# Performance work log

Hardware: AMD Instinct MI355X
Metric: run time of the kernel (lower is better)

## Reference

```python
import jax, jax.numpy as jnp
import numpy as np

NUM_NODES = 94
SEQ_LEN = 784
OUT_CLASSES = 10
ALPHA = 0.5
GAMMA = 0.1
OMEGA = 2.0 * np.pi / 28.0
H = 1.0
INV_SQRT_N = 1.0 / np.sqrt(NUM_NODES)


def _xavier(key, shape):
    fan_in, fan_out = shape[1], shape[0]
    limit = np.sqrt(6.0 / (fan_in + fan_out))
    return jax.random.uniform(key, shape, jnp.float32, -limit, limit)


def setup_inputs() -> dict:
    key = jax.random.key(0)
    k_in, k_ih, k_hh, k_ro = jax.random.split(key, 4)
    batch = 1024
    return {
        "input_sequence": jax.random.normal(k_in, (batch, SEQ_LEN), jnp.float32),
        "w_ih": _xavier(k_ih, (NUM_NODES, 1)),   # Linear(1 -> N) weight
        "b_ih": jnp.zeros((NUM_NODES,), jnp.float32),
        "w_hh": _xavier(k_hh, (NUM_NODES, NUM_NODES)),  # Linear(N -> N) weight
        "b_hh": jnp.zeros((NUM_NODES,), jnp.float32),
        "w_ro": _xavier(k_ro, (OUT_CLASSES, NUM_NODES)),  # readout weight
        "b_ro": jnp.zeros((OUT_CLASSES,), jnp.float32),
    }


def reference(input_sequence, w_ih, b_ih, w_hh, b_hh, w_ro, b_ro):
    batch = input_sequence.shape[0]
    # precompute external drive for all steps: [T, B, N]
    # W_ih(s_t) with input_dim=1 is an outer product: s_t * w_ih[:,0] + b_ih
    s = input_sequence.T  # [T, B]
    w_ih_vec = w_ih[:, 0]  # [N]

    def step(carry, s_t):
        x, y = carry
        I_ext = s_t[:, None] * w_ih_vec[None, :] + b_ih  # [B, N]
        I_rec = y @ w_hh.T + b_hh                        # [B, N]
        A = (I_ext + I_rec) * INV_SQRT_N
        accel = ALPHA * jnp.tanh(A) - 2.0 * GAMMA * y - (OMEGA ** 2) * x
        x_new = x + H * y
        y_new = y + H * accel
        return (x_new, y_new), None

    x0 = jnp.zeros((batch, NUM_NODES), jnp.float32)
    y0 = jnp.zeros((batch, NUM_NODES), jnp.float32)
    (x_final, _), _ = jax.lax.scan(step, (x0, y0), s)
    return x_final @ w_ro.T + b_ro  # [B, 10]
```

## Files before the change

### kernel.cpp

```cpp
#include <hip/hip_runtime.h>
#include <math.h>

#define NUM_NODES 94
#define SEQ_LEN 784
#define OUT_CLASSES 10
#define EPB 16
#define NW 6
#define SP 788
#define YHALF 1664

#define TWO_GAMMA 0.2f
#define OM2 0.0503551324598949f
#define INV_SQRT_N 0.103142124625879
#define LOG2E 1.4426950408889634
#define WSCALE ((float)(2.0 * INV_SQRT_N * LOG2E))

typedef _Float16 half8 __attribute__((ext_vector_type(8)));
typedef _Float16 half4 __attribute__((ext_vector_type(4)));
typedef _Float16 half2v __attribute__((ext_vector_type(2)));
typedef float    floatx4 __attribute__((ext_vector_type(4)));
typedef float    f2 __attribute__((ext_vector_type(2)));

__global__
__attribute__((amdgpu_flat_work_group_size(NW*64, NW*64)))
void horn_kernel(
    const float* __restrict__ input,
    const float* __restrict__ w_ih,
    const float* __restrict__ b_ih,
    const float* __restrict__ w_hh,
    const float* __restrict__ b_hh,
    const float* __restrict__ w_ro,
    const float* __restrict__ b_ro,
    float* __restrict__ out)
{
    __shared__ __align__(16) float    sinl[EPB * SP];
    __shared__ __align__(16) _Float16 ybuf[2][YHALF];

    const int tid  = threadIdx.x;
    const int w    = tid >> 6;
    const int lane = tid & 63;
    const int e    = lane & 15;
    const int h    = lane >> 4;
    const int bb   = blockIdx.x;

    const int  T        = w;
    const bool duty     = (w == 3 && h == 0);
    const bool tailmask = (w == 5 && h == 3);

    const int eoff = 104 * e + 4 * (e >> 3);

    {
        const floatx4* in4 = (const floatx4*)(input + (size_t)bb * EPB * SEQ_LEN);
        for (int idx = tid; idx < EPB * (SEQ_LEN / 4); idx += NW * 64) {
            int ee = idx / (SEQ_LEN / 4);
            int cc = idx - ee * (SEQ_LEN / 4);
            *(floatx4*)&sinl[ee * SP + 4 * cc] = in4[ee * (SEQ_LEN / 4) + cc];
        }
    }
    for (int i = tid; i < (2 * YHALF) / 2; i += NW * 64) ((float*)ybuf)[i] = 0.0f;

    const int arow = 16 * T + e;
    half8 a0, a1, a2;
    #pragma unroll
    for (int i = 0; i < 8; ++i) {
        const int k = 8 * h + i;
        float v0 = 0.0f, v1 = 0.0f, v2 = 0.0f;
        if (arow < NUM_NODES) {
            v0 = w_hh[arow * NUM_NODES + k] * WSCALE;
            if (k + 32 < NUM_NODES) v1 = w_hh[arow * NUM_NODES + k + 32] * WSCALE;
            const int k2 = k + 64;
            if      (k2 <  NUM_NODES) v2 = w_hh[arow * NUM_NODES + k2] * WSCALE;
            else if (k2 == NUM_NODES) v2 = w_ih[arow] * WSCALE;
            else                      v2 = (b_ih[arow] + b_hh[arow]) * WSCALE;
        }
        a0[i] = (_Float16)v0; a1[i] = (_Float16)v1; a2[i] = (_Float16)v2;
    }

    f2 x01 = {0,0}, x23 = {0,0}, y01 = {0,0}, y23 = {0,0};

    const floatx4 zf4 = {0,0,0,0};
    const f2 no2 = {-OM2, -OM2};
    const f2 p82 = {1.0f - TWO_GAMMA, 1.0f - TWO_GAMMA};
    const f2 h05 = {0.5f, 0.5f};

    __syncthreads();

    if (tid < EPB) {
        const int eo = 104 * tid + 4 * (tid >> 3);
        const float s0 = input[((size_t)bb * EPB + tid) * SEQ_LEN];
        half2v v0; v0[0] = (_Float16)s0; v0[1] = (_Float16)1.0f;
        half2v v1; v1[0] = (_Float16)0.0f; v1[1] = (_Float16)1.0f;
        *(half2v*)&ybuf[0][eo + NUM_NODES] = v0;
        *(half2v*)&ybuf[1][eo + NUM_NODES] = v1;
    }
    __syncthreads();

    #define HSTEP(RP, WP, T_) do {                                                 \
        const _Float16* Yb = &ybuf[RP][eoff + 8 * h];                              \
        half4 l0 = *(const half4*)(Yb);                                            \
        half4 u0 = *(const half4*)(Yb + 4);                                        \
        half4 l1 = *(const half4*)(Yb + 32);                                       \
        half4 u1 = *(const half4*)(Yb + 36);                                       \
        half4 l2 = *(const half4*)(Yb + 64);                                       \
        half4 u2 = *(const half4*)(Yb + 68);                                       \
                                \
        f2 q01 = no2 * x01 + h05;  q01 = p82 * y01 + q01;                          \
        f2 q23 = no2 * x23 + h05;  q23 = p82 * y23 + q23;                          \
        x01 += y01;  x23 += y23;                                                   \
        float snext = 0.0f;                                                        \
        if (duty) {                                                                \
            const int tn = ((T_) + 1 < SEQ_LEN) ? (T_) + 1 : (SEQ_LEN - 1);        \
            snext = sinl[e * SP + tn];                                             \
        }                                                                          \
        half8 B0 = __builtin_shufflevector(l0, u0, 0, 1, 2, 3, 4, 5, 6, 7);        \
        half8 B1 = __builtin_shufflevector(l1, u1, 0, 1, 2, 3, 4, 5, 6, 7);        \
        half8 B2 = __builtin_shufflevector(l2, u2, 0, 1, 2, 3, 4, 5, 6, 7);        \
        floatx4 d0 = __builtin_amdgcn_mfma_f32_16x16x32_f16(a0, B0, zf4, 0, 0, 0); \
        floatx4 d1 = __builtin_amdgcn_mfma_f32_16x16x32_f16(a1, B1, zf4, 0, 0, 0); \
        floatx4 d2 = __builtin_amdgcn_mfma_f32_16x16x32_f16(a2, B2, zf4, 0, 0, 0); \
        floatx4 d = (d0 + d1) + d2;    \
        f2 r01, r23;                                                               \
        r01[0] = __builtin_amdgcn_rcpf(__builtin_amdgcn_exp2f(d[0]) + 1.0f);       \
        r01[1] = __builtin_amdgcn_rcpf(__builtin_amdgcn_exp2f(d[1]) + 1.0f);       \
        r23[0] = __builtin_amdgcn_rcpf(__builtin_amdgcn_exp2f(d[2]) + 1.0f);       \
        r23[1] = __builtin_amdgcn_rcpf(__builtin_amdgcn_exp2f(d[3]) + 1.0f);       \
        y01 = q01 - r01;  y23 = q23 - r23;                                         \
        half4 yh;                                                                  \
        yh[0] = (_Float16)y01[0]; yh[1] = (_Float16)y01[1];                        \
        yh[2] = (_Float16)y23[0]; yh[3] = (_Float16)y23[1];                        \
        if (tailmask) {                                                            \
            half2v yt; yt[0] = yh[0]; yt[1] = yh[1];          \
            *(half2v*)&ybuf[WP][eoff + 92] = yt;                                   \
        } else {                                                                   \
            *(half4*)&ybuf[WP][eoff + 16 * T + 4 * h] = yh;                        \
        }                                                                          \
        if (duty) {                                                                \
            half2v sv; sv[0] = (_Float16)snext; sv[1] = (_Float16)1.0f;            \
            *(half2v*)&ybuf[WP][eoff + NUM_NODES] = sv;                            \
        }                                                                          \
        __syncthreads();                                                           \
    } while (0)

    for (int t = 0; t < SEQ_LEN; t += 2) {
        HSTEP(0, 1, t);
        HSTEP(1, 0, t + 1);
    }
    #undef HSTEP

    float* xsh = sinl;
    {
        floatx4 xv;
        xv[0] = x01[0]; xv[1] = x01[1]; xv[2] = x23[0]; xv[3] = x23[1];
        *(floatx4*)&xsh[e * 104 + 16 * T + 4 * h] = xv;
    }
    __syncthreads();

    if (tid < EPB * OUT_CLASSES) {
        const int ee = tid / OUT_CLASSES;
        const int c  = tid - ee * OUT_CLASSES;
        float acc = b_ro[c];
        #pragma unroll 2
        for (int r = 0; r < NUM_NODES; ++r)
            acc += xsh[ee * 104 + r] * w_ro[c * NUM_NODES + r];
        out[((size_t)bb * EPB + ee) * OUT_CLASSES + c] = acc;
    }
}

extern "C" void kernel_launch(void* const* d_in, const int* in_sizes, int n_in,
                              void* d_out, int out_size, void* d_ws, size_t ws_size,
                              hipStream_t stream) {
    const float* input = (const float*)d_in[0];
    const float* w_ih  = (const float*)d_in[1];
    const float* b_ih  = (const float*)d_in[2];
    const float* w_hh  = (const float*)d_in[3];
    const float* b_hh  = (const float*)d_in[4];
    const float* w_ro  = (const float*)d_in[5];
    const float* b_ro  = (const float*)d_in[6];
    float* out = (float*)d_out;

    const int batch = in_sizes[0] / SEQ_LEN;
    dim3 grid(batch / EPB);
    dim3 block(NW * 64);

    hipLaunchKernelGGL(horn_kernel, grid, block, 0, stream,
                       input, w_ih, b_ih, w_hh, b_hh, w_ro, b_ro, out);
}
```

Baseline: 303.4 us.

## Collapse six-wave recurrence into one wave to drop per-step barriers

The block shrinks from six waves to a single 64-lane wave that holds all six 16-row weight tiles in registers and advances all six state tiles itself. Because one wave is executed in lockstep, the y buffer no longer needs double buffering or a __syncthreads per timestep, and only a compiler memory fence remains. The three MFMAs per tile are chained through the accumulator instead of being summed afterwards, and every lane now reads the next input sample. In exchange, each wave issues six times as many MFMAs and transcendentals per step and uses more registers, so the serial per-step work grows while barrier and cross-wave LDS latency go away.

```diff
diff --git a/kernel.cpp b/kernel.cpp
--- a/kernel.cpp
+++ b/kernel.cpp
@@ -5,9 +5,8 @@
 #define SEQ_LEN 784
 #define OUT_CLASSES 10
 #define EPB 16
-#define NW 6
 #define SP 788
-#define YHALF 1664
+#define YW 100
 
 #define TWO_GAMMA 0.2f
 #define OM2 0.0503551324598949f
@@ -17,12 +16,11 @@
 
 typedef _Float16 half8 __attribute__((ext_vector_type(8)));
 typedef _Float16 half4 __attribute__((ext_vector_type(4)));
-typedef _Float16 half2v __attribute__((ext_vector_type(2)));
 typedef float    floatx4 __attribute__((ext_vector_type(4)));
 typedef float    f2 __attribute__((ext_vector_type(2)));
 
 __global__
-__attribute__((amdgpu_flat_work_group_size(NW*64, NW*64)))
+__attribute__((amdgpu_flat_work_group_size(64, 64), amdgpu_waves_per_eu(1, 4)))
 void horn_kernel(
     const float* __restrict__ input,
     const float* __restrict__ w_ih,
@@ -34,135 +32,127 @@
     float* __restrict__ out)
 {
     __shared__ __align__(16) float    sinl[EPB * SP];
-    __shared__ __align__(16) _Float16 ybuf[2][YHALF];
+    __shared__ __align__(16) _Float16 ysh[EPB * YW];
 
-    const int tid  = threadIdx.x;
-    const int w    = tid >> 6;
-    const int lane = tid & 63;
+    const int lane = threadIdx.x;
     const int e    = lane & 15;
     const int h    = lane >> 4;
     const int bb   = blockIdx.x;
 
-    const int  T        = w;
-    const bool duty     = (w == 3 && h == 0);
-    const bool tailmask = (w == 5 && h == 3);
-
-    const int eoff = 104 * e + 4 * (e >> 3);
-
     {
         const floatx4* in4 = (const floatx4*)(input + (size_t)bb * EPB * SEQ_LEN);
-        for (int idx = tid; idx < EPB * (SEQ_LEN / 4); idx += NW * 64) {
+        #pragma unroll 1
+        for (int idx = lane; idx < EPB * (SEQ_LEN / 4); idx += 64) {
             int ee = idx / (SEQ_LEN / 4);
             int cc = idx - ee * (SEQ_LEN / 4);
-            *(floatx4*)&sinl[ee * SP + 4 * cc] = in4[ee * (SEQ_LEN / 4) + cc];
+            *(floatx4*)&sinl[ee * SP + 4 * cc] = in4[idx];
         }
     }
-    for (int i = tid; i < (2 * YHALF) / 2; i += NW * 64) ((float*)ybuf)[i] = 0.0f;
 
-    const int arow = 16 * T + e;
-    half8 a0, a1, a2;
+    half8 A0[6], A1[6], A2[6];
     #pragma unroll
-    for (int i = 0; i < 8; ++i) {
-        const int k = 8 * h + i;
-        float v0 = 0.0f, v1 = 0.0f, v2 = 0.0f;
-        if (arow < NUM_NODES) {
-            v0 = w_hh[arow * NUM_NODES + k] * WSCALE;
-            if (k + 32 < NUM_NODES) v1 = w_hh[arow * NUM_NODES + k + 32] * WSCALE;
-            const int k2 = k + 64;
-            if      (k2 <  NUM_NODES) v2 = w_hh[arow * NUM_NODES + k2] * WSCALE;
-            else if (k2 == NUM_NODES) v2 = w_ih[arow] * WSCALE;
-            else                      v2 = (b_ih[arow] + b_hh[arow]) * WSCALE;
+    for (int T = 0; T < 6; ++T) {
+        const int arow = 16 * T + e;
+        #pragma unroll
+        for (int i = 0; i < 8; ++i) {
+            const int k = 8 * h + i;
+            float v0 = 0.0f, v1 = 0.0f, v2 = 0.0f;
+            if (arow < NUM_NODES) {
+                v0 = w_hh[arow * NUM_NODES + k] * WSCALE;
+                v1 = w_hh[arow * NUM_NODES + k + 32] * WSCALE;
+                const int k2 = k + 64;
+                if      (k2 <  NUM_NODES) v2 = w_hh[arow * NUM_NODES + k2] * WSCALE;
+                else if (k2 == NUM_NODES) v2 = w_ih[arow] * WSCALE;
+                else                      v2 = (b_ih[arow] + b_hh[arow]) * WSCALE;
+            }
+            A0[T][i] = (_Float16)v0; A1[T][i] = (_Float16)v1; A2[T][i] = (_Float16)v2;
         }
-        a0[i] = (_Float16)v0; a1[i] = (_Float16)v1; a2[i] = (_Float16)v2;
     }
 
-    f2 x01 = {0,0}, x23 = {0,0}, y01 = {0,0}, y23 = {0,0};
+    f2 X0[6], X1[6], Y0[6], Y1[6];
+    #pragma unroll
+    for (int T = 0; T < 6; ++T) {
+        X0[T] = (f2){0.0f, 0.0f}; X1[T] = (f2){0.0f, 0.0f};
+        Y0[T] = (f2){0.0f, 0.0f}; Y1[T] = (f2){0.0f, 0.0f};
+    }
 
-    const floatx4 zf4 = {0,0,0,0};
+    const float s0 = sinl[e * SP];
+    #pragma unroll
+    for (int T = 0; T < 6; ++T) {
+        half4 z;
+        z[0] = (_Float16)0.0f; z[1] = (_Float16)0.0f;
+        z[2] = (_Float16)0.0f; z[3] = (_Float16)0.0f;
+        if (T == 5 && h == 3) { z[2] = (_Float16)s0; z[3] = (_Float16)1.0f; }
+        *(half4*)&ysh[e * YW + 16 * T + 4 * h] = z;
+    }
+
     const f2 no2 = {-OM2, -OM2};
     const f2 p82 = {1.0f - TWO_GAMMA, 1.0f - TWO_GAMMA};
     const f2 h05 = {0.5f, 0.5f};
+    const floatx4 zf4 = {0.0f, 0.0f, 0.0f, 0.0f};
+    const _Float16* yb = &ysh[e * YW + 8 * h];
 
-    __syncthreads();
+    #pragma unroll 1
+    for (int t = 0; t < SEQ_LEN; ++t) {
+        half4 l0 = *(const half4*)(yb);
+        half4 u0 = *(const half4*)(yb + 4);
+        half4 l1 = *(const half4*)(yb + 32);
+        half4 u1 = *(const half4*)(yb + 36);
+        half4 l2 = *(const half4*)(yb + 64);
+        half4 u2 = *(const half4*)(yb + 68);
+        const int tn = (t + 1 < SEQ_LEN) ? t + 1 : (SEQ_LEN - 1);
+        float sn = sinl[e * SP + tn];
 
-    if (tid < EPB) {
-        const int eo = 104 * tid + 4 * (tid >> 3);
-        const float s0 = input[((size_t)bb * EPB + tid) * SEQ_LEN];
-        half2v v0; v0[0] = (_Float16)s0; v0[1] = (_Float16)1.0f;
-        half2v v1; v1[0] = (_Float16)0.0f; v1[1] = (_Float16)1.0f;
-        *(half2v*)&ybuf[0][eo + NUM_NODES] = v0;
-        *(half2v*)&ybuf[1][eo + NUM_NODES] = v1;
+        half8 B0 = __builtin_shufflevector(l0, u0, 0, 1, 2, 3, 4, 5, 6, 7);
+        half8 B1 = __builtin_shufflevector(l1, u1, 0, 1, 2, 3, 4, 5, 6, 7);
+        half8 B2 = __builtin_shufflevector(l2, u2, 0, 1, 2, 3, 4, 5, 6, 7);
+
+        #pragma unroll
+        for (int T = 0; T < 6; ++T) {
+            f2 q0 = no2 * X0[T] + h05;  q0 = p82 * Y0[T] + q0;
+            f2 q1 = no2 * X1[T] + h05;  q1 = p82 * Y1[T] + q1;
+            X0[T] += Y0[T];  X1[T] += Y1[T];
+            floatx4 d = __builtin_amdgcn_mfma_f32_16x16x32_f16(A0[T], B0, zf4, 0, 0, 0);
+            d = __builtin_amdgcn_mfma_f32_16x16x32_f16(A1[T], B1, d, 0, 0, 0);
+            d = __builtin_amdgcn_mfma_f32_16x16x32_f16(A2[T], B2, d, 0, 0, 0);
+            f2 r0, r1;
+            r0[0] = __builtin_amdgcn_rcpf(__builtin_amdgcn_exp2f(d[0]) + 1.0f);
+            r0[1] = __builtin_amdgcn_rcpf(__builtin_amdgcn_exp2f(d[1]) + 1.0f);
+            r1[0] = __builtin_amdgcn_rcpf(__builtin_amdgcn_exp2f(d[2]) + 1.0f);
+            r1[1] = __builtin_amdgcn_rcpf(__builtin_amdgcn_exp2f(d[3]) + 1.0f);
+            Y0[T] = q0 - r0;  Y1[T] = q1 - r1;
+            half4 yh;
+            yh[0] = (_Float16)Y0[T][0]; yh[1] = (_Float16)Y0[T][1];
+            yh[2] = (_Float16)Y1[T][0]; yh[3] = (_Float16)Y1[T][1];
+            if (T == 5 && h == 3) {
+                yh[2] = (_Float16)sn; yh[3] = (_Float16)1.0f;
+            }
+            *(half4*)&ysh[e * YW + 16 * T + 4 * h] = yh;
+        }
+        asm volatile("" ::: "memory");
     }
-    __syncthreads();
-
-    #define HSTEP(RP, WP, T_) do {                                                 \
-        const _Float16* Yb = &ybuf[RP][eoff + 8 * h];                              \
-        half4 l0 = *(const half4*)(Yb);                                            \
-        half4 u0 = *(const half4*)(Yb + 4);                                        \
-        half4 l1 = *(const half4*)(Yb + 32);                                       \
-        half4 u1 = *(const half4*)(Yb + 36);                                       \
-        half4 l2 = *(const half4*)(Yb + 64);                                       \
-        half4 u2 = *(const half4*)(Yb + 68);                                       \
-                                \
-        f2 q01 = no2 * x01 + h05;  q01 = p82 * y01 + q01;                          \
-        f2 q23 = no2 * x23 + h05;  q23 = p82 * y23 + q23;                          \
-        x01 += y01;  x23 += y23;                                                   \
-        float snext = 0.0f;                                                        \
-        if (duty) {                                                                \
-            const int tn = ((T_) + 1 < SEQ_LEN) ? (T_) + 1 : (SEQ_LEN - 1);        \
-            snext = sinl[e * SP + tn];                                             \
-        }                                                                          \
-        half8 B0 = __builtin_shufflevector(l0, u0, 0, 1, 2, 3, 4, 5, 6, 7);        \
-        half8 B1 = __builtin_shufflevector(l1, u1, 0, 1, 2, 3, 4, 5, 6, 7);        \
-        half8 B2 = __builtin_shufflevector(l2, u2, 0, 1, 2, 3, 4, 5, 6, 7);        \
-        floatx4 d0 = __builtin_amdgcn_mfma_f32_16x16x32_f16(a0, B0, zf4, 0, 0, 0); \
-        floatx4 d1 = __builtin_amdgcn_mfma_f32_16x16x32_f16(a1, B1, zf4, 0, 0, 0); \
-        floatx4 d2 = __builtin_amdgcn_mfma_f32_16x16x32_f16(a2, B2, zf4, 0, 0, 0); \
-        floatx4 d = (d0 + d1) + d2;    \
-        f2 r01, r23;                                                               \
-        r01[0] = __builtin_amdgcn_rcpf(__builtin_amdgcn_exp2f(d[0]) + 1.0f);       \
-        r01[1] = __builtin_amdgcn_rcpf(__builtin_amdgcn_exp2f(d[1]) + 1.0f);       \
-        r23[0] = __builtin_amdgcn_rcpf(__builtin_amdgcn_exp2f(d[2]) + 1.0f);       \
-        r23[1] = __builtin_amdgcn_rcpf(__builtin_amdgcn_exp2f(d[3]) + 1.0f);       \
-        y01 = q01 - r01;  y23 = q23 - r23;                                         \
-        half4 yh;                                                                  \
-        yh[0] = (_Float16)y01[0]; yh[1] = (_Float16)y01[1];                        \
-        yh[2] = (_Float16)y23[0]; yh[3] = (_Float16)y23[1];                        \
-        if (tailmask) {                                                            \
-            half2v yt; yt[0] = yh[0]; yt[1] = yh[1];          \
-            *(half2v*)&ybuf[WP][eoff + 92] = yt;                                   \
-        } else {                                                                   \
-            *(half4*)&ybuf[WP][eoff + 16 * T + 4 * h] = yh;                        \
-        }                                                                          \
-        if (duty) {                                                                \
-            half2v sv; sv[0] = (_Float16)snext; sv[1] = (_Float16)1.0f;            \
-            *(half2v*)&ybuf[WP][eoff + NUM_NODES] = sv;                            \
-        }                                                                          \
-        __syncthreads();                                                           \
-    } while (0)
-
-    for (int t = 0; t < SEQ_LEN; t += 2) {
-        HSTEP(0, 1, t);
-        HSTEP(1, 0, t + 1);
-    }
-    #undef HSTEP
 
     float* xsh = sinl;
-    {
+    #pragma unroll
+    for (int T = 0; T < 6; ++T) {
         floatx4 xv;
-        xv[0] = x01[0]; xv[1] = x01[1]; xv[2] = x23[0]; xv[3] = x23[1];
-        *(floatx4*)&xsh[e * 104 + 16 * T + 4 * h] = xv;
+        xv[0] = X0[T][0]; xv[1] = X0[T][1]; xv[2] = X1[T][0]; xv[3] = X1[T][1];
+        *(floatx4*)&xsh[e * YW + 16 * T + 4 * h] = xv;
     }
-    __syncthreads();
+    asm volatile("" ::: "memory");
 
-    if (tid < EPB * OUT_CLASSES) {
-        const int ee = tid / OUT_CLASSES;
-        const int c  = tid - ee * OUT_CLASSES;
-        float acc = b_ro[c];
-        #pragma unroll 2
-        for (int r = 0; r < NUM_NODES; ++r)
-            acc += xsh[ee * 104 + r] * w_ro[c * NUM_NODES + r];
-        out[((size_t)bb * EPB + ee) * OUT_CLASSES + c] = acc;
+    #pragma unroll 1
+    for (int k = 0; k < 3; ++k) {
+        const int idx = lane + 64 * k;
+        if (idx < EPB * OUT_CLASSES) {
+            const int ee = idx / OUT_CLASSES;
+            const int c  = idx - ee * OUT_CLASSES;
+            float acc = b_ro[c];
+            #pragma unroll 2
+            for (int r = 0; r < NUM_NODES; ++r)
+                acc += xsh[ee * YW + r] * w_ro[c * NUM_NODES + r];
+            out[((size_t)bb * EPB + ee) * OUT_CLASSES + c] = acc;
+        }
     }
 }
 
@@ -180,7 +170,7 @@
 
     const int batch = in_sizes[0] / SEQ_LEN;
     dim3 grid(batch / EPB);
-    dim3 block(NW * 64);
+    dim3 block(64);
 
     hipLaunchKernelGGL(horn_kernel, grid, block, 0, stream,
                        input, w_ih, b_ih, w_hh, b_hh, w_ro, b_ro, out);
```

Measured after the change: 549.2 us. 81.0% more time.

## Interleave two independent 16-element recurrence chains per block with in-place LDS state

Applied to the files above, without the earlier changes.

Each block now handles 32 batch elements as two independent 16-element chains. One chain's MFMA and activation math is interleaved with the other chain's LDS reads, with a barrier between them, to hide barrier and LDS latency in the serial time loop. The double-buffered state is replaced by one in-place buffer per chain. The input sequence is staged into shared memory in two halves so it fits in LDS. This halves the grid, so fewer CUs are in use, and each barrier interval now carries serial work for both chains.

```diff
diff --git a/kernel.cpp b/kernel.cpp
--- a/kernel.cpp
+++ b/kernel.cpp
@@ -4,10 +4,11 @@
 #define NUM_NODES 94
 #define SEQ_LEN 784
 #define OUT_CLASSES 10
-#define EPB 16
+#define EPB 32
 #define NW 6
-#define SP 788
-#define YHALF 1664
+#define SP 396
+#define THALF 392
+#define YCH 1664
 
 #define TWO_GAMMA 0.2f
 #define OM2 0.0503551324598949f
@@ -34,7 +35,7 @@
     float* __restrict__ out)
 {
     __shared__ __align__(16) float    sinl[EPB * SP];
-    __shared__ __align__(16) _Float16 ybuf[2][YHALF];
+    __shared__ __align__(16) _Float16 ysh[2][YCH];
 
     const int tid  = threadIdx.x;
     const int w    = tid >> 6;
@@ -44,114 +45,136 @@
     const int bb   = blockIdx.x;
 
     const int  T        = w;
-    const bool duty     = (w == 3 && h == 0);
     const bool tailmask = (w == 5 && h == 3);
+    const bool dutyA    = (w == 3 && h == 0);
+    const bool dutyB    = (w == 2 && h == 0);
+    const int  sElA     = e;
+    const int  sElB     = 16 + e;
 
     const int eoff = 104 * e + 4 * (e >> 3);
 
-    {
-        const floatx4* in4 = (const floatx4*)(input + (size_t)bb * EPB * SEQ_LEN);
-        for (int idx = tid; idx < EPB * (SEQ_LEN / 4); idx += NW * 64) {
-            int ee = idx / (SEQ_LEN / 4);
-            int cc = idx - ee * (SEQ_LEN / 4);
-            *(floatx4*)&sinl[ee * SP + 4 * cc] = in4[ee * (SEQ_LEN / 4) + cc];
-        }
-    }
-    for (int i = tid; i < (2 * YHALF) / 2; i += NW * 64) ((float*)ybuf)[i] = 0.0f;
+    for (int i = tid; i < (2 * YCH) / 2; i += NW * 64) ((float*)ysh)[i] = 0.0f;
+    __syncthreads();
+    if (tid < EPB) {
+        const int c  = tid >> 4, ee = tid & 15;
+        const int eo = 104 * ee + 4 * (ee >> 3);
+        const float s0 = input[((size_t)bb * EPB + tid) * SEQ_LEN];
+        half2v v; v[0] = (_Float16)s0; v[1] = (_Float16)1.0f;
+        *(half2v*)&ysh[c][eo + NUM_NODES] = v;
+    }
+    __syncthreads();
 
     const int arow = 16 * T + e;
-    half8 a0, a1, a2;
+    half8 A0, A1, A2;
     #pragma unroll
     for (int i = 0; i < 8; ++i) {
         const int k = 8 * h + i;
         float v0 = 0.0f, v1 = 0.0f, v2 = 0.0f;
         if (arow < NUM_NODES) {
             v0 = w_hh[arow * NUM_NODES + k] * WSCALE;
-            if (k + 32 < NUM_NODES) v1 = w_hh[arow * NUM_NODES + k + 32] * WSCALE;
+            v1 = w_hh[arow * NUM_NODES + k + 32] * WSCALE;
             const int k2 = k + 64;
             if      (k2 <  NUM_NODES) v2 = w_hh[arow * NUM_NODES + k2] * WSCALE;
             else if (k2 == NUM_NODES) v2 = w_ih[arow] * WSCALE;
             else                      v2 = (b_ih[arow] + b_hh[arow]) * WSCALE;
         }
-        a0[i] = (_Float16)v0; a1[i] = (_Float16)v1; a2[i] = (_Float16)v2;
-    }
-
-    f2 x01 = {0,0}, x23 = {0,0}, y01 = {0,0}, y23 = {0,0};
-
-    const floatx4 zf4 = {0,0,0,0};
+        A0[i] = (_Float16)v0; A1[i] = (_Float16)v1; A2[i] = (_Float16)v2;
+    }
+
+    f2 X0[2], X1[2], Y0[2], Y1[2];
+    #pragma unroll
+    for (int c = 0; c < 2; ++c) {
+        X0[c] = (f2){0,0}; X1[c] = (f2){0,0};
+        Y0[c] = (f2){0,0}; Y1[c] = (f2){0,0};
+    }
+
+    half4 L0[2], U0[2], L1[2], U1[2], L2[2], U2[2];
+
     const f2 no2 = {-OM2, -OM2};
     const f2 p82 = {1.0f - TWO_GAMMA, 1.0f - TWO_GAMMA};
     const f2 h05 = {0.5f, 0.5f};
-
-    __syncthreads();
-
-    if (tid < EPB) {
-        const int eo = 104 * tid + 4 * (tid >> 3);
-        const float s0 = input[((size_t)bb * EPB + tid) * SEQ_LEN];
-        half2v v0; v0[0] = (_Float16)s0; v0[1] = (_Float16)1.0f;
-        half2v v1; v1[0] = (_Float16)0.0f; v1[1] = (_Float16)1.0f;
-        *(half2v*)&ybuf[0][eo + NUM_NODES] = v0;
-        *(half2v*)&ybuf[1][eo + NUM_NODES] = v1;
-    }
-    __syncthreads();
-
-    #define HSTEP(RP, WP, T_) do {                                                 \
-        const _Float16* Yb = &ybuf[RP][eoff + 8 * h];                              \
-        half4 l0 = *(const half4*)(Yb);                                            \
-        half4 u0 = *(const half4*)(Yb + 4);                                        \
-        half4 l1 = *(const half4*)(Yb + 32);                                       \
-        half4 u1 = *(const half4*)(Yb + 36);                                       \
-        half4 l2 = *(const half4*)(Yb + 64);                                       \
-        half4 u2 = *(const half4*)(Yb + 68);                                       \
-                                \
-        f2 q01 = no2 * x01 + h05;  q01 = p82 * y01 + q01;                          \
-        f2 q23 = no2 * x23 + h05;  q23 = p82 * y23 + q23;                          \
-        x01 += y01;  x23 += y23;                                                   \
-        float snext = 0.0f;                                                        \
-        if (duty) {                                                                \
-            const int tn = ((T_) + 1 < SEQ_LEN) ? (T_) + 1 : (SEQ_LEN - 1);        \
-            snext = sinl[e * SP + tn];                                             \
+    const floatx4 zf4 = {0,0,0,0};
+
+    #define READC(C) do {                                                          \
+        const _Float16* yb = &ysh[(C)][eoff + 8 * h];                              \
+        L0[C] = *(const half4*)(yb);      U0[C] = *(const half4*)(yb + 4);         \
+        L1[C] = *(const half4*)(yb + 32); U1[C] = *(const half4*)(yb + 36);        \
+        L2[C] = *(const half4*)(yb + 64); U2[C] = *(const half4*)(yb + 68);        \
+    } while (0)
+
+    #define COMPC(C, DUTY, SEL) do {                                               \
+        f2 q0 = no2 * X0[C] + h05;  q0 = p82 * Y0[C] + q0;                         \
+        f2 q1 = no2 * X1[C] + h05;  q1 = p82 * Y1[C] + q1;                         \
+        X0[C] += Y0[C];  X1[C] += Y1[C];                                           \
+        float sn = 0.0f;                                                           \
+        if (DUTY) {                                                                \
+            if (tl + 1 < THALF) sn = sinl[(SEL) * SP + tl + 1];                    \
+            else {                                                                 \
+                const int tg = (t + 1 < SEQ_LEN) ? t + 1 : (SEQ_LEN - 1);          \
+                sn = input[((size_t)bb * EPB + (SEL)) * SEQ_LEN + tg];             \
+            }                                                                      \
         }                                                                          \
-        half8 B0 = __builtin_shufflevector(l0, u0, 0, 1, 2, 3, 4, 5, 6, 7);        \
-        half8 B1 = __builtin_shufflevector(l1, u1, 0, 1, 2, 3, 4, 5, 6, 7);        \
-        half8 B2 = __builtin_shufflevector(l2, u2, 0, 1, 2, 3, 4, 5, 6, 7);        \
-        floatx4 d0 = __builtin_amdgcn_mfma_f32_16x16x32_f16(a0, B0, zf4, 0, 0, 0); \
-        floatx4 d1 = __builtin_amdgcn_mfma_f32_16x16x32_f16(a1, B1, zf4, 0, 0, 0); \
-        floatx4 d2 = __builtin_amdgcn_mfma_f32_16x16x32_f16(a2, B2, zf4, 0, 0, 0); \
-        floatx4 d = (d0 + d1) + d2;    \
-        f2 r01, r23;                                                               \
-        r01[0] = __builtin_amdgcn_rcpf(__builtin_amdgcn_exp2f(d[0]) + 1.0f);       \
-        r01[1] = __builtin_amdgcn_rcpf(__builtin_amdgcn_exp2f(d[1]) + 1.0f);       \
-        r23[0] = __builtin_amdgcn_rcpf(__builtin_amdgcn_exp2f(d[2]) + 1.0f);       \
-        r23[1] = __builtin_amdgcn_rcpf(__builtin_amdgcn_exp2f(d[3]) + 1.0f);       \
-        y01 = q01 - r01;  y23 = q23 - r23;                                         \
+        half8 B0 = __builtin_shufflevector(L0[C], U0[C], 0,1,2,3,4,5,6,7);         \
+        half8 B1 = __builtin_shufflevector(L1[C], U1[C], 0,1,2,3,4,5,6,7);         \
+        half8 B2 = __builtin_shufflevector(L2[C], U2[C], 0,1,2,3,4,5,6,7);         \
+        floatx4 d  = __builtin_amdgcn_mfma_f32_16x16x32_f16(A0, B0, zf4, 0, 0, 0); \
+        floatx4 dp = __builtin_amdgcn_mfma_f32_16x16x32_f16(A1, B1, zf4, 0, 0, 0); \
+        d = __builtin_amdgcn_mfma_f32_16x16x32_f16(A2, B2, d, 0, 0, 0);            \
+        d += dp;                                                                   \
+        f2 r0, r1;                                                                 \
+        r0[0] = __builtin_amdgcn_rcpf(__builtin_amdgcn_exp2f(d[0]) + 1.0f);        \
+        r0[1] = __builtin_amdgcn_rcpf(__builtin_amdgcn_exp2f(d[1]) + 1.0f);        \
+        r1[0] = __builtin_amdgcn_rcpf(__builtin_amdgcn_exp2f(d[2]) + 1.0f);        \
+        r1[1] = __builtin_amdgcn_rcpf(__builtin_amdgcn_exp2f(d[3]) + 1.0f);        \
+        Y0[C] = q0 - r0;  Y1[C] = q1 - r1;                                         \
         half4 yh;                                                                  \
-        yh[0] = (_Float16)y01[0]; yh[1] = (_Float16)y01[1];                        \
-        yh[2] = (_Float16)y23[0]; yh[3] = (_Float16)y23[1];                        \
+        yh[0] = (_Float16)Y0[C][0]; yh[1] = (_Float16)Y0[C][1];                    \
+        yh[2] = (_Float16)Y1[C][0]; yh[3] = (_Float16)Y1[C][1];                    \
         if (tailmask) {                                                            \
-            half2v yt; yt[0] = yh[0]; yt[1] = yh[1];          \
-            *(half2v*)&ybuf[WP][eoff + 92] = yt;                                   \
+            half2v yt; yt[0] = yh[0]; yt[1] = yh[1];                               \
+            *(half2v*)&ysh[C][eoff + 92] = yt;                                     \
         } else {                                                                   \
-            *(half4*)&ybuf[WP][eoff + 16 * T + 4 * h] = yh;                        \
+            *(half4*)&ysh[C][eoff + 16 * T + 4 * h] = yh;                          \
         }                                                                          \
-        if (duty) {                                                                \
-            half2v sv; sv[0] = (_Float16)snext; sv[1] = (_Float16)1.0f;            \
-            *(half2v*)&ybuf[WP][eoff + NUM_NODES] = sv;                            \
+        if (DUTY) {                                                                \
+            half2v sv; sv[0] = (_Float16)sn; sv[1] = (_Float16)1.0f;               \
+            *(half2v*)&ysh[C][eoff + NUM_NODES] = sv;                              \
         }                                                                          \
-        __syncthreads();                                                           \
     } while (0)
 
-    for (int t = 0; t < SEQ_LEN; t += 2) {
-        HSTEP(0, 1, t);
-        HSTEP(1, 0, t + 1);
-    }
-    #undef HSTEP
+    READC(0);
+
+    for (int hf = 0; hf < 2; ++hf) {
+        {
+            const float* src = input + (size_t)bb * EPB * SEQ_LEN + hf * THALF;
+            for (int idx = tid; idx < EPB * (THALF / 4); idx += NW * 64) {
+                int ee = idx / (THALF / 4);
+                int cc = idx - ee * (THALF / 4);
+                *(floatx4*)&sinl[ee * SP + 4 * cc] =
+                    *(const floatx4*)(src + (size_t)ee * SEQ_LEN + 4 * cc);
+            }
+        }
+        __syncthreads();
+
+        for (int tl = 0; tl < THALF; ++tl) {
+            const int t = hf * THALF + tl;
+            COMPC(0, dutyA, sElA);
+            READC(1);
+            __syncthreads();
+            COMPC(1, dutyB, sElB);
+            READC(0);
+            __syncthreads();
+        }
+    }
+    #undef COMPC
+    #undef READC
 
     float* xsh = sinl;
-    {
+    #pragma unroll
+    for (int c = 0; c < 2; ++c) {
         floatx4 xv;
-        xv[0] = x01[0]; xv[1] = x01[1]; xv[2] = x23[0]; xv[3] = x23[1];
-        *(floatx4*)&xsh[e * 104 + 16 * T + 4 * h] = xv;
+        xv[0] = X0[c][0]; xv[1] = X0[c][1]; xv[2] = X1[c][0]; xv[3] = X1[c][1];
+        *(floatx4*)&xsh[(16 * c + e) * 100 + 16 * T + 4 * h] = xv;
     }
     __syncthreads();
 
@@ -161,7 +184,7 @@
         float acc = b_ro[c];
         #pragma unroll 2
         for (int r = 0; r < NUM_NODES; ++r)
-            acc += xsh[ee * 104 + r] * w_ro[c * NUM_NODES + r];
+            acc += xsh[ee * 100 + r] * w_ro[c * NUM_NODES + r];
         out[((size_t)bb * EPB + ee) * OUT_CLASSES + c] = acc;
     }
 }
```

Result: slower. 552.4 us (+82.1%).

## Shrink block to four waves with shared redundant row-tile computation

Applied to the files above, without the earlier changes.

Cuts the workgroup from six wavefronts to four. Each wave now owns one private 16-row tile and computes one of two extra tiles redundantly with another wave. Only half of each duplicated tile gets published, chosen by wave parity. The aim is to make each per-step barrier cheaper by having fewer waves to sync, and to use 16-byte LDS reads without padding. The cost is doubled MFMA and transcendental work per wave and duplicated recurrence state.

```diff
diff --git a/kernel.cpp b/kernel.cpp
--- a/kernel.cpp
+++ b/kernel.cpp
@@ -5,9 +5,9 @@
 #define SEQ_LEN 784
 #define OUT_CLASSES 10
 #define EPB 16
-#define NW 6
+#define NW 4
 #define SP 788
-#define YHALF 1664
+#define YP 104
 
 #define TWO_GAMMA 0.2f
 #define OM2 0.0503551324598949f
@@ -34,7 +34,7 @@
     float* __restrict__ out)
 {
     __shared__ __align__(16) float    sinl[EPB * SP];
-    __shared__ __align__(16) _Float16 ybuf[2][YHALF];
+    __shared__ __align__(16) _Float16 ybuf[2][EPB * YP];
 
     const int tid  = threadIdx.x;
     const int w    = tid >> 6;
@@ -43,100 +43,114 @@
     const int h    = lane >> 4;
     const int bb   = blockIdx.x;
 
-    const int  T        = w;
-    const bool duty     = (w == 3 && h == 0);
-    const bool tailmask = (w == 5 && h == 3);
-
-    const int eoff = 104 * e + 4 * (e >> 3);
+    const int  S      = 4 + (w >> 1);
+    const int  sthalf = w & 1;
+    const bool shpub  = ((h >> 1) == sthalf);
+    const bool duty   = (w == 0 && h == 3);
+    const bool tail53 = (w == 3 && h == 3);
 
     {
         const floatx4* in4 = (const floatx4*)(input + (size_t)bb * EPB * SEQ_LEN);
         for (int idx = tid; idx < EPB * (SEQ_LEN / 4); idx += NW * 64) {
             int ee = idx / (SEQ_LEN / 4);
             int cc = idx - ee * (SEQ_LEN / 4);
-            *(floatx4*)&sinl[ee * SP + 4 * cc] = in4[ee * (SEQ_LEN / 4) + cc];
+            *(floatx4*)&sinl[ee * SP + 4 * cc] = in4[idx];
         }
     }
-    for (int i = tid; i < (2 * YHALF) / 2; i += NW * 64) ((float*)ybuf)[i] = 0.0f;
-
-    const int arow = 16 * T + e;
-    half8 a0, a1, a2;
-    #pragma unroll
-    for (int i = 0; i < 8; ++i) {
-        const int k = 8 * h + i;
-        float v0 = 0.0f, v1 = 0.0f, v2 = 0.0f;
-        if (arow < NUM_NODES) {
-            v0 = w_hh[arow * NUM_NODES + k] * WSCALE;
-            if (k + 32 < NUM_NODES) v1 = w_hh[arow * NUM_NODES + k + 32] * WSCALE;
-            const int k2 = k + 64;
-            if      (k2 <  NUM_NODES) v2 = w_hh[arow * NUM_NODES + k2] * WSCALE;
-            else if (k2 == NUM_NODES) v2 = w_ih[arow] * WSCALE;
-            else                      v2 = (b_ih[arow] + b_hh[arow]) * WSCALE;
-        }
-        a0[i] = (_Float16)v0; a1[i] = (_Float16)v1; a2[i] = (_Float16)v2;
-    }
-
-    f2 x01 = {0,0}, x23 = {0,0}, y01 = {0,0}, y23 = {0,0};
-
-    const floatx4 zf4 = {0,0,0,0};
+    for (int i = tid; i < (2 * EPB * YP) / 2; i += NW * 64) ((float*)ybuf)[i] = 0.0f;
+    __syncthreads();
+    if (tid < EPB) {
+        const float s0 = sinl[tid * SP];
+        half2v v; v[0] = (_Float16)s0; v[1] = (_Float16)1.0f;
+        *(half2v*)&ybuf[0][tid * YP + NUM_NODES] = v;
+    }
+    __syncthreads();
+
+    #define LOAD_A(ROW, A0, A1, A2) do {                                           \
+        const int arow = (ROW);                                                    \
+        _Pragma("unroll")                                                          \
+        for (int i = 0; i < 8; ++i) {                                              \
+            const int k = 8 * h + i;                                               \
+            float v0 = 0.0f, v1 = 0.0f, v2 = 0.0f;                                 \
+            if (arow < NUM_NODES) {                                                \
+                v0 = w_hh[arow * NUM_NODES + k] * WSCALE;                          \
+                v1 = w_hh[arow * NUM_NODES + k + 32] * WSCALE;                     \
+                const int k2 = k + 64;                                             \
+                if      (k2 <  NUM_NODES) v2 = w_hh[arow * NUM_NODES + k2] * WSCALE; \
+                else if (k2 == NUM_NODES) v2 = w_ih[arow] * WSCALE;                \
+                else                      v2 = (b_ih[arow] + b_hh[arow]) * WSCALE; \
+            }                                                                      \
+            (A0)[i] = (_Float16)v0; (A1)[i] = (_Float16)v1; (A2)[i] = (_Float16)v2;\
+        }                                                                          \
+    } while (0)
+
+    half8 AO0, AO1, AO2, AS0, AS1, AS2;
+    LOAD_A(16 * w + e, AO0, AO1, AO2);
+    LOAD_A(16 * S + e, AS0, AS1, AS2);
+    #undef LOAD_A
+
+    f2 xo01 = {0,0}, xo23 = {0,0}, yo01 = {0,0}, yo23 = {0,0};
+    f2 xs01 = {0,0}, xs23 = {0,0}, ys01 = {0,0}, ys23 = {0,0};
+
     const f2 no2 = {-OM2, -OM2};
     const f2 p82 = {1.0f - TWO_GAMMA, 1.0f - TWO_GAMMA};
     const f2 h05 = {0.5f, 0.5f};
-
-    __syncthreads();
-
-    if (tid < EPB) {
-        const int eo = 104 * tid + 4 * (tid >> 3);
-        const float s0 = input[((size_t)bb * EPB + tid) * SEQ_LEN];
-        half2v v0; v0[0] = (_Float16)s0; v0[1] = (_Float16)1.0f;
-        half2v v1; v1[0] = (_Float16)0.0f; v1[1] = (_Float16)1.0f;
-        *(half2v*)&ybuf[0][eo + NUM_NODES] = v0;
-        *(half2v*)&ybuf[1][eo + NUM_NODES] = v1;
-    }
-    __syncthreads();
+    const floatx4 zf4 = {0,0,0,0};
 
     #define HSTEP(RP, WP, T_) do {                                                 \
-        const _Float16* Yb = &ybuf[RP][eoff + 8 * h];                              \
-        half4 l0 = *(const half4*)(Yb);                                            \
-        half4 u0 = *(const half4*)(Yb + 4);                                        \
-        half4 l1 = *(const half4*)(Yb + 32);                                       \
-        half4 u1 = *(const half4*)(Yb + 36);                                       \
-        half4 l2 = *(const half4*)(Yb + 64);                                       \
-        half4 u2 = *(const half4*)(Yb + 68);                                       \
-                                \
-        f2 q01 = no2 * x01 + h05;  q01 = p82 * y01 + q01;                          \
-        f2 q23 = no2 * x23 + h05;  q23 = p82 * y23 + q23;                          \
-        x01 += y01;  x23 += y23;                                                   \
-        float snext = 0.0f;                                                        \
+        const _Float16* yb = &ybuf[RP][e * YP + 8 * h];                            \
+        half8 B0 = *(const half8*)(yb);                                            \
+        half8 B1 = *(const half8*)(yb + 32);                                       \
+        half8 B2 = *(const half8*)(yb + 64);                                       \
+        float sn = 0.0f;                                                           \
         if (duty) {                                                                \
             const int tn = ((T_) + 1 < SEQ_LEN) ? (T_) + 1 : (SEQ_LEN - 1);        \
-            snext = sinl[e * SP + tn];                                             \
-        }                                                                          \
-        half8 B0 = __builtin_shufflevector(l0, u0, 0, 1, 2, 3, 4, 5, 6, 7);        \
-        half8 B1 = __builtin_shufflevector(l1, u1, 0, 1, 2, 3, 4, 5, 6, 7);        \
-        half8 B2 = __builtin_shufflevector(l2, u2, 0, 1, 2, 3, 4, 5, 6, 7);        \
-        floatx4 d0 = __builtin_amdgcn_mfma_f32_16x16x32_f16(a0, B0, zf4, 0, 0, 0); \
-        floatx4 d1 = __builtin_amdgcn_mfma_f32_16x16x32_f16(a1, B1, zf4, 0, 0, 0); \
-        floatx4 d2 = __builtin_amdgcn_mfma_f32_16x16x32_f16(a2, B2, zf4, 0, 0, 0); \
-        floatx4 d = (d0 + d1) + d2;    \
-        f2 r01, r23;                                                               \
-        r01[0] = __builtin_amdgcn_rcpf(__builtin_amdgcn_exp2f(d[0]) + 1.0f);       \
-        r01[1] = __builtin_amdgcn_rcpf(__builtin_amdgcn_exp2f(d[1]) + 1.0f);       \
-        r23[0] = __builtin_amdgcn_rcpf(__builtin_amdgcn_exp2f(d[2]) + 1.0f);       \
-        r23[1] = __builtin_amdgcn_rcpf(__builtin_amdgcn_exp2f(d[3]) + 1.0f);       \
-        y01 = q01 - r01;  y23 = q23 - r23;                                         \
+            sn = sinl[e * SP + tn];                                                \
+        }                                                                          \
+                         \
+        f2 qo0 = no2 * xo01 + h05;  qo0 = p82 * yo01 + qo0;                        \
+        f2 qo1 = no2 * xo23 + h05;  qo1 = p82 * yo23 + qo1;                        \
+        f2 qs0 = no2 * xs01 + h05;  qs0 = p82 * ys01 + qs0;                        \
+        f2 qs1 = no2 * xs23 + h05;  qs1 = p82 * ys23 + qs1;                        \
+        xo01 += yo01;  xo23 += yo23;  xs01 += ys01;  xs23 += ys23;                 \
+                                    \
+        floatx4 dO  = __builtin_amdgcn_mfma_f32_16x16x32_f16(AO0, B0, zf4, 0, 0, 0); \
+        floatx4 dOp = __builtin_amdgcn_mfma_f32_16x16x32_f16(AO1, B1, zf4, 0, 0, 0); \
+        floatx4 dS  = __builtin_amdgcn_mfma_f32_16x16x32_f16(AS0, B0, zf4, 0, 0, 0); \
+        floatx4 dSp = __builtin_amdgcn_mfma_f32_16x16x32_f16(AS1, B1, zf4, 0, 0, 0); \
+        dO = __builtin_amdgcn_mfma_f32_16x16x32_f16(AO2, B2, dO, 0, 0, 0);         \
+        dS = __builtin_amdgcn_mfma_f32_16x16x32_f16(AS2, B2, dS, 0, 0, 0);         \
+        dO += dOp;  dS += dSp;                          \
+        f2 r0, r1;                                                                 \
+        r0[0] = __builtin_amdgcn_rcpf(__builtin_amdgcn_exp2f(dO[0]) + 1.0f);       \
+        r0[1] = __builtin_amdgcn_rcpf(__builtin_amdgcn_exp2f(dO[1]) + 1.0f);       \
+        r1[0] = __builtin_amdgcn_rcpf(__builtin_amdgcn_exp2f(dO[2]) + 1.0f);       \
+        r1[1] = __builtin_amdgcn_rcpf(__builtin_amdgcn_exp2f(dO[3]) + 1.0f);       \
+        yo01 = qo0 - r0;  yo23 = qo1 - r1;                                         \
         half4 yh;                                                                  \
-        yh[0] = (_Float16)y01[0]; yh[1] = (_Float16)y01[1];                        \
-        yh[2] = (_Float16)y23[0]; yh[3] = (_Float16)y23[1];                        \
-        if (tailmask) {                                                            \
-            half2v yt; yt[0] = yh[0]; yt[1] = yh[1];          \
-            *(half2v*)&ybuf[WP][eoff + 92] = yt;                                   \
-        } else {                                                                   \
-            *(half4*)&ybuf[WP][eoff + 16 * T + 4 * h] = yh;                        \
+        yh[0] = (_Float16)yo01[0]; yh[1] = (_Float16)yo01[1];                      \
+        yh[2] = (_Float16)yo23[0]; yh[3] = (_Float16)yo23[1];                      \
+        *(half4*)&ybuf[WP][e * YP + 16 * w + 4 * h] = yh;       \
+        f2 s0_, s1_;                                                               \
+        s0_[0] = __builtin_amdgcn_rcpf(__builtin_amdgcn_exp2f(dS[0]) + 1.0f);      \
+        s0_[1] = __builtin_amdgcn_rcpf(__builtin_amdgcn_exp2f(dS[1]) + 1.0f);      \
+        s1_[0] = __builtin_amdgcn_rcpf(__builtin_amdgcn_exp2f(dS[2]) + 1.0f);      \
+        s1_[1] = __builtin_amdgcn_rcpf(__builtin_amdgcn_exp2f(dS[3]) + 1.0f);      \
+        ys01 = qs0 - s0_;  ys23 = qs1 - s1_;                                       \
+        half4 yhs;                                                                 \
+        yhs[0] = (_Float16)ys01[0]; yhs[1] = (_Float16)ys01[1];                    \
+        yhs[2] = (_Float16)ys23[0]; yhs[3] = (_Float16)ys23[1];                    \
+        if (shpub) {                                                               \
+            if (tail53) {                                                          \
+                half2v yt; yt[0] = yhs[0]; yt[1] = yhs[1];         \
+                *(half2v*)&ybuf[WP][e * YP + 92] = yt;                             \
+            } else {                                                               \
+                *(half4*)&ybuf[WP][e * YP + 16 * S + 4 * h] = yhs;                 \
+            }                                                                      \
         }                                                                          \
         if (duty) {                                                                \
-            half2v sv; sv[0] = (_Float16)snext; sv[1] = (_Float16)1.0f;            \
-            *(half2v*)&ybuf[WP][eoff + NUM_NODES] = sv;                            \
+            half2v sv; sv[0] = (_Float16)sn; sv[1] = (_Float16)1.0f;               \
+            *(half2v*)&ybuf[WP][e * YP + NUM_NODES] = sv;                          \
         }                                                                          \
         __syncthreads();                                                           \
     } while (0)
@@ -150,8 +164,13 @@
     float* xsh = sinl;
     {
         floatx4 xv;
-        xv[0] = x01[0]; xv[1] = x01[1]; xv[2] = x23[0]; xv[3] = x23[1];
-        *(floatx4*)&xsh[e * 104 + 16 * T + 4 * h] = xv;
+        xv[0] = xo01[0]; xv[1] = xo01[1]; xv[2] = xo23[0]; xv[3] = xo23[1];
+        *(floatx4*)&xsh[e * 100 + 16 * w + 4 * h] = xv;
+        if (shpub) {
+            floatx4 xw;
+            xw[0] = xs01[0]; xw[1] = xs01[1]; xw[2] = xs23[0]; xw[3] = xs23[1];
+            *(floatx4*)&xsh[e * 100 + 16 * S + 4 * h] = xw;
+        }
     }
     __syncthreads();
 
@@ -161,7 +180,7 @@
         float acc = b_ro[c];
         #pragma unroll 2
         for (int r = 0; r < NUM_NODES; ++r)
-            acc += xsh[ee * 104 + r] * w_ro[c * NUM_NODES + r];
+            acc += xsh[ee * 100 + r] * w_ro[c * NUM_NODES + r];
         out[((size_t)bb * EPB + ee) * OUT_CLASSES + c] = acc;
     }
 }
```

Measured after the change: 344.6 us. 13.6% more time.
